# Optimization experiments

Measured on AMD Instinct MI355X. Metric: run time of the kernel, lower is better.

The kernel has to match this reference:

```python
import jax, jax.numpy as jnp
import numpy as np
from jax.scipy.linalg import solve_triangular

L_SUB = 16          # subarray length (init arg L)
DL = 0.05           # diagonal loading factor


def setup_inputs() -> dict:
    key = jax.random.key(0)
    k0, k1, k2 = jax.random.split(key, 3)
    B, C, NS, NZ, NX = 2, 128, 1024, 256, 128
    rf = jax.random.normal(k0, (B, C, NS), jnp.float32)
    t0 = jnp.zeros((B,), jnp.float32)
    d_tx = jax.random.uniform(k1, (B, NZ, NX), dtype=jnp.float32)
    d_rx = jax.random.uniform(k2, (C, NZ, NX), dtype=jnp.float32)
    fs = jnp.float32((NS - 1) / 2.0)   # keeps sample positions in [0, NS-1]
    f0 = jnp.float32(5.0)              # unused by forward (kept for signature parity)
    c0 = jnp.float32(1.0)
    apod = jnp.ones((C,), jnp.float32) # unused by forward
    return dict(rf=rf, t0=t0, d_tx=d_tx, d_rx=d_rx, fs=fs, f0=f0, c0=c0, apod=apod)


def _aligned_signals(rf, t0, d_tx, d_rx, fs, c0):
    """Bilinear (1-D linear) resample of rf at per-pixel delays.
    Equivalent to torch grid_sample(mode='bilinear', padding_mode='border',
    align_corners=True) where the grid x-coord is samples*2/(NS-1)-1."""
    B, C, NS = rf.shape
    _, NZ, NX = d_tx.shape
    # samples: [B, C, NZ, NX] fractional sample index into rf
    samples = fs * ((d_tx[:, None, :, :] + d_rx[None, :, :, :]) / c0
                    + t0[:, None, None, None])
    pos = jnp.clip(samples, 0.0, NS - 1.0)          # border padding
    i0 = jnp.floor(pos).astype(jnp.int32)
    i1 = jnp.minimum(i0 + 1, NS - 1)
    frac = pos - i0.astype(pos.dtype)
    sig = rf.reshape(B * C, NS)
    i0f = i0.reshape(B * C, NZ * NX)
    i1f = i1.reshape(B * C, NZ * NX)
    v0 = jnp.take_along_axis(sig, i0f, axis=1).reshape(B, C, NZ, NX)
    v1 = jnp.take_along_axis(sig, i1f, axis=1).reshape(B, C, NZ, NX)
    return v0 * (1.0 - frac) + v1 * frac


def reference(rf, t0, d_tx, d_rx, fs, f0, c0, apod):
    B, C, NS = rf.shape
    _, NZ, NX = d_tx.shape
    M = C - L_SUB + 1  # number of subarrays (113)
    aligned = _aligned_signals(rf, t0, d_tx, d_rx, fs, c0)  # [B, C, NZ, NX]
    # per-pixel channel vectors: [P, C], P = B*NZ*NX
    xf = aligned.transpose(0, 2, 3, 1).reshape(-1, C)
    # subarray gather: S[p, m, l] = xf[p, m + l]  -> [P, M, L]
    idx = jnp.arange(M)[:, None] + jnp.arange(L_SUB)[None, :]
    S = xf[:, idx]
    # avg_pool1d(kernel=M, stride=1) over channels == mean over subarray axis
    x = S.mean(axis=1)                                  # [P, L]
    # spatially-smoothed covariance: R = S^T S / M, symmetrized
    R = jnp.einsum('pml,pmk->plk', S, S) / M
    R = 0.5 * (R + R.transpose(0, 2, 1))
    # diagonal loading: R += dl * (trace/L) * I
    delta = jnp.trace(R, axis1=-2, axis2=-1) / L_SUB    # [P]
    R = R + (DL * delta)[:, None, None] * jnp.eye(L_SUB, dtype=R.dtype)
    # Cholesky solve R u = 1
    Lc = jnp.linalg.cholesky(R)
    rhs = jnp.ones((R.shape[0], L_SUB, 1), R.dtype)
    y1 = solve_triangular(Lc, rhs, lower=True)
    u = solve_triangular(Lc, y1, lower=True, trans=1)[..., 0]  # [P, L]
    # MVDR weights (steering a = ones) and beamformed output
    denom = jnp.sum(u, axis=-1, keepdims=True) + 1e-10
    w = u / denom
    y = jnp.sum(w * x, axis=-1)                         # [P]
    return y.reshape(B, NZ, NX)
```

## Files before the change

### kernel.cpp

```cpp
#include <hip/hip_runtime.h>


namespace {

constexpr int kB  = 2;
constexpr int kC  = 128;
constexpr int kNS = 1024;
constexpr int kNZ = 256;
constexpr int kNX = 128;
constexpr int kZX = kNZ * kNX;
constexpr int kChunk = 8;
constexpr int kChunkF = kChunk * kNS;
constexpr int kTPB = 128;

__device__ __host__ constexpr int tri(int l, int k) {
  return l * 16 - (l * (l - 1)) / 2 + (k - l);
}

typedef __attribute__((address_space(1))) const void gconst_t;
typedef __attribute__((address_space(3))) void ldsv_t;

__device__ __forceinline__ void g2l16(const float* g, float* l) {
  __builtin_amdgcn_global_load_lds((gconst_t*)g, (ldsv_t*)l, 16, 0, 0);
}

__device__ __forceinline__ void stage_chunk(const float* __restrict__ gsrc,
                                            float* ldst, int woff, int lane) {
#pragma unroll
  for (int i = 0; i < 16; ++i)
    g2l16(gsrc + woff + i * 256 + lane * 4, ldst + woff + i * 256);
}

__device__ __forceinline__ void load_drx(const float* __restrict__ drx_px,
                                         int cbase, float (&d)[kChunk]) {
#pragma unroll
  for (int r = 0; r < kChunk; ++r)
    d[r] = drx_px[(size_t)(cbase + r) * kZX];
}

template <int PH, bool HEAD>
__device__ __forceinline__ void chunk_compute(
    const float* rows, const float (&drx)[kChunk], float kk, float base,
    float (&F)[16], float (&win)[16], float (&head)[16], float& Sall) {
#pragma unroll
  for (int r = 0; r < kChunk; ++r) {
    const int t = PH + r;
    float pos = fmaf(kk, drx[r], base);
    pos = fminf(fmaxf(pos, 0.0f), 1023.0f);
    int i0 = (int)pos;
    i0 = min(i0, kNS - 2);
    float frac = pos - (float)i0;
    const float* p = rows + r * kNS + i0;
    float v0 = p[0];
    float v1 = p[1];
    float v = fmaf(frac, v1 - v0, v0);
    Sall += v;
    F[0] = fmaf(v, v, F[0]);
    if constexpr (HEAD) {
#pragma unroll
      for (int d = 1; d <= t; ++d) F[d] = fmaf(v, win[t - d], F[d]);
      head[t] = v;
    } else {
#pragma unroll
      for (int d = 1; d < 16; ++d) F[d] = fmaf(v, win[(t - d) & 15], F[d]);
    }
    win[t] = v;
  }
}

__global__ __launch_bounds__(kTPB, 1) void mvb_fused_kernel(
    const float* __restrict__ rf, const float* __restrict__ t0,
    const float* __restrict__ d_tx, const float* __restrict__ d_rx,
    const float* __restrict__ fs_p, const float* __restrict__ c0_p,
    float* __restrict__ out) {
  __shared__ float tile[2 * kChunkF];

  const int tid = threadIdx.x;
  const int lane = tid & 63;
  const int wave = tid >> 6;
  const int woff = wave * 4096;
  const int z = blockIdx.x & (kNZ - 1);
  const int b = blockIdx.x >> 8;
  const int x = tid;
  const int pix = (int)((size_t)b * kZX + z * kNX + x);

  const float fs = fs_p[0];
  const float c0 = c0_p[0];
  const float kk = fs / c0;
  const float base = fs * (d_tx[pix] / c0 + t0[b]);

  const float* rfb = rf + (size_t)b * kC * kNS;
  const float* drx_px = d_rx + (size_t)z * kNX + x;

  float F[16], win[16], head[16];
  float Sall = 0.0f;
#pragma unroll
  for (int i = 0; i < 16; ++i) F[i] = 0.0f;

  float drx0[kChunk], drx1[kChunk];

  stage_chunk(rfb, tile, woff, lane);
  load_drx(drx_px, 0, drx0);
  __syncthreads();

  stage_chunk(rfb + kChunkF, tile + kChunkF, woff, lane);
  load_drx(drx_px, 8, drx1);
  chunk_compute<0, true>(tile, drx0, kk, base, F, win, head, Sall);
  __syncthreads();

  stage_chunk(rfb + 2 * kChunkF, tile, woff, lane);
  load_drx(drx_px, 16, drx0);
  chunk_compute<8, true>(tile + kChunkF, drx1, kk, base, F, win, head, Sall);
  __syncthreads();

  for (int g = 0; g < 7; ++g) {
    const int q0 = 2 * g + 2;
    stage_chunk(rfb + (size_t)(q0 + 1) * kChunkF, tile + kChunkF, woff, lane);
    load_drx(drx_px, (q0 + 1) * kChunk, drx1);
    chunk_compute<0, false>(tile, drx0, kk, base, F, win, head, Sall);
    __syncthreads();

    if (q0 + 2 < 16) {
      stage_chunk(rfb + (size_t)(q0 + 2) * kChunkF, tile, woff, lane);
      load_drx(drx_px, (q0 + 2) * kChunk, drx0);
    }
    chunk_compute<8, false>(tile + kChunkF, drx1, kk, base, F, win, head,
                            Sall);
    __syncthreads();
  }

  float Ru[136];
#pragma unroll
  for (int d = 0; d < 16; ++d) {
    float t0s = 0.0f;
#pragma unroll
    for (int i = d + 1; i < 16; ++i) t0s = fmaf(win[i - d], win[i], t0s);
    Ru[tri(0, d)] = F[d] - t0s;
#pragma unroll
    for (int l = 1; l < 16 - d; ++l)
      Ru[tri(l, l + d)] = Ru[tri(l - 1, l - 1 + d)] -
                          head[l - 1] * head[l - 1 + d] +
                          win[l] * win[l + d];
  }

  float tr = 0.0f;
#pragma unroll
  for (int l = 0; l < 16; ++l) tr += Ru[tri(l, l)];
  const float dl = tr * (0.05f / 16.0f);
#pragma unroll
  for (int l = 0; l < 16; ++l) Ru[tri(l, l)] += dl;

  float X[16];
  {
    float s = Sall;
#pragma unroll
    for (int i = 1; i < 16; ++i) s -= win[i];
    X[0] = s;
#pragma unroll
    for (int l = 1; l < 16; ++l) X[l] = X[l - 1] - head[l - 1] + win[l];
  }

  float inv[16];
#pragma unroll
  for (int j = 0; j < 16; ++j) {
    float d = Ru[tri(j, j)];
#pragma unroll
    for (int p = 0; p < j; ++p) d = fmaf(-Ru[tri(p, j)], Ru[tri(p, j)], d);
    inv[j] = rsqrtf(d);
#pragma unroll
    for (int i = j + 1; i < 16; ++i) {
      float s = Ru[tri(j, i)];
#pragma unroll
      for (int p = 0; p < j; ++p) s = fmaf(-Ru[tri(p, i)], Ru[tri(p, j)], s);
      Ru[tri(j, i)] = s * inv[j];
    }
  }

  float yv[16];
#pragma unroll
  for (int i = 0; i < 16; ++i) {
    float s = 1.0f;
#pragma unroll
    for (int j = 0; j < i; ++j) s = fmaf(-Ru[tri(j, i)], yv[j], s);
    yv[i] = s * inv[i];
  }
  float u[16];
#pragma unroll
  for (int i = 15; i >= 0; --i) {
    float s = yv[i];
#pragma unroll
    for (int j = i + 1; j < 16; ++j) s = fmaf(-Ru[tri(i, j)], u[j], s);
    u[i] = s * inv[i];
  }

  float su = 0.0f, dot = 0.0f;
#pragma unroll
  for (int i = 0; i < 16; ++i) {
    su += u[i];
    dot = fmaf(u[i], X[i], dot);
  }
  out[pix] = dot / (113.0f * su + 1e-10f);
}

}

extern "C" void kernel_launch(void* const* d_in, const int* in_sizes, int n_in,
                              void* d_out, int out_size, void* d_ws,
                              size_t ws_size, hipStream_t stream) {
  const float* rf   = (const float*)d_in[0];
  const float* t0   = (const float*)d_in[1];
  const float* d_tx = (const float*)d_in[2];
  const float* d_rx = (const float*)d_in[3];
  const float* fs   = (const float*)d_in[4];
  const float* c0   = (const float*)d_in[6];
  float* out = (float*)d_out;

  hipLaunchKernelGGL(mvb_fused_kernel, dim3(kB * kNZ), dim3(kTPB), 0, stream,
                     rf, t0, d_tx, d_rx, fs, c0, out);
}
```

Baseline: 95.44 us.

## Split channel accumulation across two thread halves and merge lag sums via LDS

Each pixel's 128 channels are now split into two halves of 64, processed by separate 128-thread groups in a 256-thread block, with 4-row double-buffered LDS stages. After accumulation, the lower half writes its lag products, window and head to LDS, and the upper half merges them, adding cross-boundary lag terms, before running the Cholesky solve alone. The aim is to double the waves per block and shorten each thread's serial channel loop so latency is hidden better. The cost is an extra LDS exchange, idle lower-half threads during the solve, and more synchronisation steps.

New measurement: 97.66 us. +2.3%, slower.

```diff
diff --git a/kernel.cpp b/kernel.cpp
--- a/kernel.cpp
+++ b/kernel.cpp
@@ -9,9 +9,10 @@
 constexpr int kNZ = 256;
 constexpr int kNX = 128;
 constexpr int kZX = kNZ * kNX;
-constexpr int kChunk = 8;
-constexpr int kChunkF = kChunk * kNS;
-constexpr int kTPB = 128;
+constexpr int kHalfC = 64;
+constexpr int kRows = 4;
+constexpr int kBufF = 2 * kRows * kNS;
+constexpr int kTPB = 256;
 
 __device__ __host__ constexpr int tri(int l, int k) {
   return l * 16 - (l * (l - 1)) / 2 + (k - l);
@@ -24,26 +25,31 @@
   __builtin_amdgcn_global_load_lds((gconst_t*)g, (ldsv_t*)l, 16, 0, 0);
 }
 
-__device__ __forceinline__ void stage_chunk(const float* __restrict__ gsrc,
-                                            float* ldst, int woff, int lane) {
-#pragma unroll
-  for (int i = 0; i < 16; ++i)
+__device__ __forceinline__ void stage_step(const float* __restrict__ rfb,
+                                           float* tbuf, int q, int wave,
+                                           int lane) {
+  const int h = wave >> 1;
+  const int woff = (wave & 1) * 2048;
+  const float* gsrc = rfb + (size_t)(h * kHalfC + q * kRows) * kNS;
+  float* ldst = tbuf + h * (kRows * kNS);
+#pragma unroll
+  for (int i = 0; i < 8; ++i)
     g2l16(gsrc + woff + i * 256 + lane * 4, ldst + woff + i * 256);
 }
 
-__device__ __forceinline__ void load_drx(const float* __restrict__ drx_px,
-                                         int cbase, float (&d)[kChunk]) {
-#pragma unroll
-  for (int r = 0; r < kChunk; ++r)
-    d[r] = drx_px[(size_t)(cbase + r) * kZX];
+__device__ __forceinline__ void load_drx4(const float* __restrict__ drxp,
+                                          int cbase, float (&d)[kRows]) {
+#pragma unroll
+  for (int r = 0; r < kRows; ++r)
+    d[r] = drxp[(size_t)(cbase + r) * kZX];
 }
 
 template <int PH, bool HEAD>
-__device__ __forceinline__ void chunk_compute(
-    const float* rows, const float (&drx)[kChunk], float kk, float base,
+__device__ __forceinline__ void compute4(
+    const float* rows, const float (&drx)[kRows], float kk, float base,
     float (&F)[16], float (&win)[16], float (&head)[16], float& Sall) {
 #pragma unroll
-  for (int r = 0; r < kChunk; ++r) {
+  for (int r = 0; r < kRows; ++r) {
     const int t = PH + r;
     float pos = fmaf(kk, drx[r], base);
     pos = fminf(fmaxf(pos, 0.0f), 1023.0f);
@@ -68,21 +74,32 @@
   }
 }
 
-__global__ __launch_bounds__(kTPB, 1) void mvb_fused_kernel(
+#define STEP(Q, PH, HEADF, CUR, NXT)                                       \
+  do {                                                                     \
+    if ((Q) + 1 < 16) {                                                    \
+      stage_step(rfb, tile[((Q) + 1) & 1], (Q) + 1, wave, lane);           \
+      load_drx4(drxp, ((Q) + 1) * kRows, NXT);                             \
+    }                                                                      \
+    compute4<PH, HEADF>(tile[(Q) & 1] + half * (kRows * kNS), CUR, kk,     \
+                        base, F, win, head, Sall);                         \
+    __syncthreads();                                                       \
+  } while (0)
+
+__global__ __launch_bounds__(kTPB, 2) void mvb_fused_kernel(
     const float* __restrict__ rf, const float* __restrict__ t0,
     const float* __restrict__ d_tx, const float* __restrict__ d_rx,
     const float* __restrict__ fs_p, const float* __restrict__ c0_p,
     float* __restrict__ out) {
-  __shared__ float tile[2 * kChunkF];
+  __shared__ float tile[2][kBufF];
 
   const int tid = threadIdx.x;
   const int lane = tid & 63;
   const int wave = tid >> 6;
-  const int woff = wave * 4096;
+  const int half = tid >> 7;
+  const int px = tid & 127;
   const int z = blockIdx.x & (kNZ - 1);
   const int b = blockIdx.x >> 8;
-  const int x = tid;
-  const int pix = (int)((size_t)b * kZX + z * kNX + x);
+  const int pix = (int)((size_t)b * kZX + z * kNX + px);
 
   const float fs = fs_p[0];
   const float c0 = c0_p[0];
@@ -90,43 +107,62 @@
   const float base = fs * (d_tx[pix] / c0 + t0[b]);
 
   const float* rfb = rf + (size_t)b * kC * kNS;
-  const float* drx_px = d_rx + (size_t)z * kNX + x;
+  const float* drxp =
+      d_rx + (size_t)half * kHalfC * kZX + (size_t)z * kNX + px;
 
   float F[16], win[16], head[16];
   float Sall = 0.0f;
 #pragma unroll
   for (int i = 0; i < 16; ++i) F[i] = 0.0f;
 
-  float drx0[kChunk], drx1[kChunk];
-
-  stage_chunk(rfb, tile, woff, lane);
-  load_drx(drx_px, 0, drx0);
+  float drxA[kRows], drxB[kRows];
+
+  stage_step(rfb, tile[0], 0, wave, lane);
+  load_drx4(drxp, 0, drxA);
   __syncthreads();
 
-  stage_chunk(rfb + kChunkF, tile + kChunkF, woff, lane);
-  load_drx(drx_px, 8, drx1);
-  chunk_compute<0, true>(tile, drx0, kk, base, F, win, head, Sall);
+  STEP(0, 0, true, drxA, drxB);
+  STEP(1, 4, true, drxB, drxA);
+  STEP(2, 8, true, drxA, drxB);
+  STEP(3, 12, true, drxB, drxA);
+#pragma unroll 1
+  for (int g = 1; g < 4; ++g) {
+    const int q = g * 4;
+    STEP(q + 0, 0, false, drxA, drxB);
+    STEP(q + 1, 4, false, drxB, drxA);
+    STEP(q + 2, 8, false, drxA, drxB);
+    STEP(q + 3, 12, false, drxB, drxA);
+  }
+
+  float* xch = tile[0];
+  if (half == 0) {
+#pragma unroll
+    for (int i = 0; i < 16; ++i) xch[i * 128 + px] = F[i];
+#pragma unroll
+    for (int i = 0; i < 16; ++i) xch[(16 + i) * 128 + px] = win[i];
+#pragma unroll
+    for (int i = 0; i < 16; ++i) xch[(32 + i) * 128 + px] = head[i];
+    xch[48 * 128 + px] = Sall;
+  }
   __syncthreads();
-
-  stage_chunk(rfb + 2 * kChunkF, tile, woff, lane);
-  load_drx(drx_px, 16, drx0);
-  chunk_compute<8, true>(tile + kChunkF, drx1, kk, base, F, win, head, Sall);
-  __syncthreads();
-
-  for (int g = 0; g < 7; ++g) {
-    const int q0 = 2 * g + 2;
-    stage_chunk(rfb + (size_t)(q0 + 1) * kChunkF, tile + kChunkF, woff, lane);
-    load_drx(drx_px, (q0 + 1) * kChunk, drx1);
-    chunk_compute<0, false>(tile, drx0, kk, base, F, win, head, Sall);
-    __syncthreads();
-
-    if (q0 + 2 < 16) {
-      stage_chunk(rfb + (size_t)(q0 + 2) * kChunkF, tile, woff, lane);
-      load_drx(drx_px, (q0 + 2) * kChunk, drx0);
+  if (half == 0) return;
+
+  float hlo[16];
+  {
+    float wlo[16];
+#pragma unroll
+    for (int i = 0; i < 16; ++i) wlo[i] = xch[(16 + i) * 128 + px];
+#pragma unroll
+    for (int i = 0; i < 16; ++i) hlo[i] = xch[(32 + i) * 128 + px];
+    Sall += xch[48 * 128 + px];
+    F[0] += xch[0 * 128 + px];
+#pragma unroll
+    for (int d = 1; d < 16; ++d) {
+      float s = xch[d * 128 + px];
+#pragma unroll
+      for (int i = 0; i < d; ++i) s = fmaf(head[i], wlo[16 - d + i], s);
+      F[d] += s;
     }
-    chunk_compute<8, false>(tile + kChunkF, drx1, kk, base, F, win, head,
-                            Sall);
-    __syncthreads();
   }
 
   float Ru[136];
@@ -139,7 +175,7 @@
 #pragma unroll
     for (int l = 1; l < 16 - d; ++l)
       Ru[tri(l, l + d)] = Ru[tri(l - 1, l - 1 + d)] -
-                          head[l - 1] * head[l - 1 + d] +
+                          hlo[l - 1] * hlo[l - 1 + d] +
                           win[l] * win[l + d];
   }
 
@@ -157,7 +193,7 @@
     for (int i = 1; i < 16; ++i) s -= win[i];
     X[0] = s;
 #pragma unroll
-    for (int l = 1; l < 16; ++l) X[l] = X[l - 1] - head[l - 1] + win[l];
+    for (int l = 1; l < 16; ++l) X[l] = X[l - 1] - hlo[l - 1] + win[l];
   }
 
   float inv[16];
```

## Replace LDS-staged rf tiles with direct global gathers and two rows per block

Applied to the files above, without the earlier changes.

Removes the double-buffered LDS staging of rf chunks and the per-chunk barriers. Each thread now gathers its two interpolation samples directly from global memory (8-byte loads, relying on L1/L2 to cache rf), processing 16 channels per step. Blocks now cover two z rows with 256 threads and half as many blocks are launched. This trades guaranteed LDS-local gathers for cache-dependent scattered global loads, while dropping the synchronisation and staging bandwidth.

Measured after the change: 94.92 us (median of 2 runs). Within noise of the previous version (-0.5%).

```diff
diff --git a/kernel.cpp b/kernel.cpp
--- a/kernel.cpp
+++ b/kernel.cpp
@@ -9,79 +9,59 @@
 constexpr int kNZ = 256;
 constexpr int kNX = 128;
 constexpr int kZX = kNZ * kNX;
-constexpr int kChunk = 8;
-constexpr int kChunkF = kChunk * kNS;
-constexpr int kTPB = 128;
+constexpr int kTPB = 256;
 
 __device__ __host__ constexpr int tri(int l, int k) {
   return l * 16 - (l * (l - 1)) / 2 + (k - l);
 }
 
-typedef __attribute__((address_space(1))) const void gconst_t;
-typedef __attribute__((address_space(3))) void ldsv_t;
+template <bool HEAD>
+__device__ __forceinline__ void chunk16(
+    const float* __restrict__ rfq,
+    const float* __restrict__ drxp, int cbase, float kk, float base,
+    float (&F)[16], float (&win)[16], float (&head)[16], float& Sall) {
+  float dr[16];
+#pragma unroll
+  for (int r = 0; r < 16; ++r) dr[r] = drxp[(size_t)(cbase + r) * kZX];
 
-__device__ __forceinline__ void g2l16(const float* g, float* l) {
-  __builtin_amdgcn_global_load_lds((gconst_t*)g, (ldsv_t*)l, 16, 0, 0);
-}
-
-__device__ __forceinline__ void stage_chunk(const float* __restrict__ gsrc,
-                                            float* ldst, int woff, int lane) {
+  float2 vv[16];
+  float fr[16];
 #pragma unroll
-  for (int i = 0; i < 16; ++i)
-    g2l16(gsrc + woff + i * 256 + lane * 4, ldst + woff + i * 256);
-}
-
-__device__ __forceinline__ void load_drx(const float* __restrict__ drx_px,
-                                         int cbase, float (&d)[kChunk]) {
-#pragma unroll
-  for (int r = 0; r < kChunk; ++r)
-    d[r] = drx_px[(size_t)(cbase + r) * kZX];
-}
-
-template <int PH, bool HEAD>
-__device__ __forceinline__ void chunk_compute(
-    const float* rows, const float (&drx)[kChunk], float kk, float base,
-    float (&F)[16], float (&win)[16], float (&head)[16], float& Sall) {
-#pragma unroll
-  for (int r = 0; r < kChunk; ++r) {
-    const int t = PH + r;
-    float pos = fmaf(kk, drx[r], base);
+  for (int r = 0; r < 16; ++r) {
+    float pos = fmaf(kk, dr[r], base);
     pos = fminf(fmaxf(pos, 0.0f), 1023.0f);
     int i0 = (int)pos;
     i0 = min(i0, kNS - 2);
-    float frac = pos - (float)i0;
-    const float* p = rows + r * kNS + i0;
-    float v0 = p[0];
-    float v1 = p[1];
-    float v = fmaf(frac, v1 - v0, v0);
+    fr[r] = pos - (float)i0;
+    __builtin_memcpy(&vv[r], rfq + r * kNS + i0, 8);
+  }
+
+#pragma unroll
+  for (int r = 0; r < 16; ++r) {
+    float v = fmaf(fr[r], vv[r].y - vv[r].x, vv[r].x);
     Sall += v;
     F[0] = fmaf(v, v, F[0]);
     if constexpr (HEAD) {
 #pragma unroll
-      for (int d = 1; d <= t; ++d) F[d] = fmaf(v, win[t - d], F[d]);
-      head[t] = v;
+      for (int d = 1; d <= r; ++d) F[d] = fmaf(v, win[r - d], F[d]);
+      head[r] = v;
     } else {
 #pragma unroll
-      for (int d = 1; d < 16; ++d) F[d] = fmaf(v, win[(t - d) & 15], F[d]);
+      for (int d = 1; d < 16; ++d) F[d] = fmaf(v, win[(r - d) & 15], F[d]);
     }
-    win[t] = v;
+    win[r] = v;
   }
 }
 
-__global__ __launch_bounds__(kTPB, 1) void mvb_fused_kernel(
+__global__ __launch_bounds__(kTPB, 1) void mvb_kernel(
     const float* __restrict__ rf, const float* __restrict__ t0,
     const float* __restrict__ d_tx, const float* __restrict__ d_rx,
     const float* __restrict__ fs_p, const float* __restrict__ c0_p,
     float* __restrict__ out) {
-  __shared__ float tile[2 * kChunkF];
-
   const int tid = threadIdx.x;
-  const int lane = tid & 63;
-  const int wave = tid >> 6;
-  const int woff = wave * 4096;
-  const int z = blockIdx.x & (kNZ - 1);
-  const int b = blockIdx.x >> 8;
-  const int x = tid;
+  const int b = blockIdx.x >> 7;
+  const int z = ((blockIdx.x & 127) << 1) + (tid >> 7);
+  const int x = tid & 127;
   const int pix = (int)((size_t)b * kZX + z * kNX + x);
 
   const float fs = fs_p[0];
@@ -90,44 +70,18 @@
   const float base = fs * (d_tx[pix] / c0 + t0[b]);
 
   const float* rfb = rf + (size_t)b * kC * kNS;
-  const float* drx_px = d_rx + (size_t)z * kNX + x;
+  const float* drxp = d_rx + (size_t)z * kNX + x;
 
   float F[16], win[16], head[16];
   float Sall = 0.0f;
 #pragma unroll
   for (int i = 0; i < 16; ++i) F[i] = 0.0f;
 
-  float drx0[kChunk], drx1[kChunk];
-
-  stage_chunk(rfb, tile, woff, lane);
-  load_drx(drx_px, 0, drx0);
-  __syncthreads();
-
-  stage_chunk(rfb + kChunkF, tile + kChunkF, woff, lane);
-  load_drx(drx_px, 8, drx1);
-  chunk_compute<0, true>(tile, drx0, kk, base, F, win, head, Sall);
-  __syncthreads();
-
-  stage_chunk(rfb + 2 * kChunkF, tile, woff, lane);
-  load_drx(drx_px, 16, drx0);
-  chunk_compute<8, true>(tile + kChunkF, drx1, kk, base, F, win, head, Sall);
-  __syncthreads();
-
-  for (int g = 0; g < 7; ++g) {
-    const int q0 = 2 * g + 2;
-    stage_chunk(rfb + (size_t)(q0 + 1) * kChunkF, tile + kChunkF, woff, lane);
-    load_drx(drx_px, (q0 + 1) * kChunk, drx1);
-    chunk_compute<0, false>(tile, drx0, kk, base, F, win, head, Sall);
-    __syncthreads();
-
-    if (q0 + 2 < 16) {
-      stage_chunk(rfb + (size_t)(q0 + 2) * kChunkF, tile, woff, lane);
-      load_drx(drx_px, (q0 + 2) * kChunk, drx0);
-    }
-    chunk_compute<8, false>(tile + kChunkF, drx1, kk, base, F, win, head,
-                            Sall);
-    __syncthreads();
-  }
+  chunk16<true>(rfb, drxp, 0, kk, base, F, win, head, Sall);
+#pragma unroll 1
+  for (int q = 1; q < 8; ++q)
+    chunk16<false>(rfb + (size_t)q * 16 * kNS, drxp, q * 16, kk, base, F, win,
+                   head, Sall);
 
   float Ru[136];
 #pragma unroll
@@ -215,6 +169,6 @@
   const float* c0   = (const float*)d_in[6];
   float* out = (float*)d_out;
 
-  hipLaunchKernelGGL(mvb_fused_kernel, dim3(kB * kNZ), dim3(kTPB), 0, stream,
+  hipLaunchKernelGGL(mvb_kernel, dim3(kB * kNZ / 2), dim3(kTPB), 0, stream,
                      rf, t0, d_tx, d_rx, fs, c0, out);
 }
```
